# Kernel optimization log

Measured on AMD Instinct MI355X. Metric: run time of the kernel, lower is better.

The kernel has to match this reference:

```python
import jax, jax.numpy as jnp
import numpy as np

N = 50000
E = 1600000
D_IN = 256
D_OUT = 256
NUM_SAMPLES = 5
LN_EPS = 1e-5


def setup_inputs() -> dict:
    key = jax.random.key(0)
    ks = jax.random.split(key, 6)
    x = jax.random.normal(ks[0], (N, D_IN), dtype=jnp.float32)
    adj_indices = jax.random.randint(ks[1], (2, E), 0, N, dtype=jnp.int32)
    adj_values = jax.random.uniform(ks[2], (E,), dtype=jnp.float32)
    mask = jax.random.uniform(ks[3], (NUM_SAMPLES, D_OUT), dtype=jnp.float32)
    # Xavier-uniform init as in reset_parameters
    limit_w = float(np.sqrt(6.0 / (D_IN + D_OUT)))
    weight = jax.random.uniform(ks[4], (D_IN, D_OUT), dtype=jnp.float32,
                                minval=-limit_w, maxval=limit_w)
    limit_b = float(np.sqrt(6.0 / (1 + D_OUT)))
    bias = jax.random.uniform(ks[5], (1, D_OUT), dtype=jnp.float32,
                              minval=-limit_b, maxval=limit_b)
    ln_gamma = jnp.ones((D_OUT,), dtype=jnp.float32)
    ln_beta = jnp.zeros((D_OUT,), dtype=jnp.float32)
    return {"x": x, "adj_indices": adj_indices, "adj_values": adj_values,
            "mask": mask, "weight": weight, "bias": bias,
            "ln_gamma": ln_gamma, "ln_beta": ln_beta}


def reference(x, adj_indices, adj_values, mask, weight, bias, ln_gamma, ln_beta):
    # dense transform: [N, D_in] @ [D_in, D_out]
    h = x @ weight
    # sparse adjacency spmm (COO): out[r] += v_e * h[c] for each edge e=(r,c)
    rows, cols = adj_indices[0], adj_indices[1]
    h = jax.ops.segment_sum(adj_values[:, None] * h[cols], rows, num_segments=N)
    # bias + ELU
    h = jax.nn.elu(h + bias)
    # LayerNorm over feature dim
    mu = jnp.mean(h, axis=-1, keepdims=True)
    var = jnp.var(h, axis=-1, keepdims=True)
    h = (h - mu) * jax.lax.rsqrt(var + LN_EPS) * ln_gamma + ln_beta
    # expand to num_samples and apply per-sample mask: [N, S, D_out]
    out = h[:, None, :] * mask[None, :, :]
    return out
```

## Files before the change

### kernel.cpp

```cpp
#include <hip/hip_runtime.h>
#include <math.h>

#define NNODES 50000
#define D 256
#define NSAMP 5
#define LN_EPS 1e-5f
#define NB 196
#define BCAP 9216
#define ACHUNK 8192

typedef __bf16 bf16;
typedef __attribute__((ext_vector_type(8))) __bf16 bf16x8;
typedef __attribute__((ext_vector_type(4))) float f32x4;
typedef unsigned long long u64;
typedef unsigned int u32;

__device__ inline float bflo(u32 u) { return __uint_as_float(u << 16); }
__device__ inline float bfhi(u32 u) { return __uint_as_float(u & 0xffff0000u); }

__device__ inline u64 packrec(int r, int c, float v) {
    return (u64)(u32)(c | (r << 16)) | ((u64)__float_as_uint(v) << 32);
}

__global__ __launch_bounds__(256) void prep_t_kernel(const float* __restrict__ w,
                                                     bf16* __restrict__ wt) {
    __shared__ float t[64][65];
    const int bi = blockIdx.x >> 2;
    const int bj = blockIdx.x & 3;
    const int tid = threadIdx.x;
#pragma unroll
    for (int it = 0; it < 16; ++it) {
        const int krow = (tid >> 6) + it * 4;
        const int ncol = tid & 63;
        t[krow][ncol] = w[(size_t)(bi * 64 + krow) * D + (bj * 64 + ncol)];
    }
    __syncthreads();
#pragma unroll
    for (int it = 0; it < 16; ++it) {
        const int nrow = (tid >> 6) + it * 4;
        const int kcol = tid & 63;
        wt[(size_t)(bj * 64 + nrow) * D + (bi * 64 + kcol)] = (bf16)t[kcol][nrow];
    }
}

__global__ __launch_bounds__(256) void gemm_binA_kernel(const float* __restrict__ x,
                                                        const bf16* __restrict__ wt,
                                                        bf16* __restrict__ h,
                                                        const int* __restrict__ rows,
                                                        const int* __restrict__ cols,
                                                        const float* __restrict__ vals,
                                                        int* __restrict__ bcur,
                                                        u64* __restrict__ binned,
                                                        int AB, int E) {
    if ((int)blockIdx.x < AB) {
        __shared__ int hist[NB];
        __shared__ int base[NB];
        for (int i = threadIdx.x; i < NB; i += 256) hist[i] = 0;
        __syncthreads();
        const int e0 = blockIdx.x * ACHUNK;
        const int e1 = min(e0 + ACHUNK, E);
        for (int e = e0 + threadIdx.x; e < e1; e += 256)
            atomicAdd(&hist[rows[e] >> 8], 1);
        __syncthreads();
        for (int i = threadIdx.x; i < NB; i += 256) {
            const int c = hist[i];
            base[i] = c ? atomicAdd(&bcur[i], c) : 0;
            hist[i] = 0;
        }
        __syncthreads();
        for (int e = e0 + threadIdx.x; e < e1; e += 256) {
            const int r = rows[e];
            const int b = r >> 8;
            const int k = base[b] + atomicAdd(&hist[b], 1);
            if (k < BCAP)
                binned[(size_t)b * BCAP + k] = packrec(r, cols[e], vals[e]);
        }
        return;
    }

    const int gb = blockIdx.x - AB;
    const int wave = threadIdx.x >> 6;
    const int lane = threadIdx.x & 63;
    const int row0 = gb * 64 + wave * 16;
    const int am = lane & 15;
    const int ag = lane >> 4;

    int arow = row0 + am;
    if (arow >= NNODES) arow = NNODES - 1;

    f32x4 acc[16];
#pragma unroll
    for (int n = 0; n < 16; ++n) acc[n] = (f32x4){0.f, 0.f, 0.f, 0.f};

#pragma unroll
    for (int kk = 0; kk < 8; ++kk) {
        const int kb = kk * 32 + ag * 8;
        const float* xp = x + (size_t)arow * D + kb;
        const f32x4 a0 = __builtin_nontemporal_load((const f32x4*)xp);
        const f32x4 a1 = __builtin_nontemporal_load((const f32x4*)(xp + 4));
        bf16x8 a;
        a[0] = (bf16)a0[0]; a[1] = (bf16)a0[1]; a[2] = (bf16)a0[2]; a[3] = (bf16)a0[3];
        a[4] = (bf16)a1[0]; a[5] = (bf16)a1[1]; a[6] = (bf16)a1[2]; a[7] = (bf16)a1[3];
#pragma unroll
        for (int n = 0; n < 16; ++n) {
            const bf16x8 b = *(const bf16x8*)(wt + (size_t)(n * 16 + am) * D + kb);
            acc[n] = __builtin_amdgcn_mfma_f32_16x16x32_bf16(a, b, acc[n], 0, 0, 0);
        }
    }

    const int drow = row0 + ag * 4;
#pragma unroll
    for (int r = 0; r < 4; ++r) {
        if (drow + r < NNODES) {
            bf16* hp = h + (size_t)(drow + r) * D + am;
#pragma unroll
            for (int n = 0; n < 16; ++n) hp[n * 16] = (bf16)acc[n][r];
        }
    }
}

__global__ __launch_bounds__(256) void sortB_kernel(const u64* __restrict__ binned,
                                                    const int* __restrict__ bcur,
                                                    u32* __restrict__ sorted,
                                                    int* __restrict__ rstart,
                                                    int* __restrict__ rcnt) {
    const int b = blockIdx.x;
    const int tid = threadIdx.x;
    const int cnt_b = min(bcur[b], BCAP);
    const u64* src = binned + (size_t)b * BCAP;

    __shared__ int hist[256];
    __shared__ int scn[256];
    hist[tid] = 0;
    __syncthreads();
    for (int i = tid; i < cnt_b; i += 256)
        atomicAdd(&hist[(int)((src[i] >> 16) & 255)], 1);
    __syncthreads();
    const int v = hist[tid];
    scn[tid] = v;
    __syncthreads();
    for (int d = 1; d < 256; d <<= 1) {
        const int t = (tid >= d) ? scn[tid - d] : 0;
        __syncthreads();
        scn[tid] += t;
        __syncthreads();
    }
    const int excl = scn[tid] - v;
    const int r = b * 256 + tid;
    if (r < NNODES) {
        rstart[r] = b * BCAP + excl;
        rcnt[r]   = v;
    }
    hist[tid] = excl;
    __syncthreads();
    for (int i = tid; i < cnt_b; i += 256) {
        const u64 rec = src[i];
        const int k = atomicAdd(&hist[(int)((rec >> 16) & 255)], 1);
        const float vf = __uint_as_float((u32)(rec >> 32));
        const u32 vb = __float_as_uint((float)(bf16)vf) & 0xffff0000u;
        sorted[(size_t)b * BCAP + k] = (u32)(rec & 0xFFFF) | vb;
    }
}

__global__ __launch_bounds__(256) void row_kernel(const unsigned short* __restrict__ hb,
                                                  const int* __restrict__ rstart,
                                                  const int* __restrict__ rcnt,
                                                  const u32* __restrict__ ep,
                                                  const float* __restrict__ bias,
                                                  const float* __restrict__ gamma,
                                                  const float* __restrict__ beta,
                                                  const float* __restrict__ mask,
                                                  float* __restrict__ out, int n) {
    const int wave = threadIdx.x >> 6;
    const int lane = threadIdx.x & 63;
    const int r = blockIdx.x * 4 + wave;
    if (r >= n) return;

    const int s = rstart[r];
    const int e = s + rcnt[r];

    float a0 = 0.f, a1 = 0.f, a2 = 0.f, a3 = 0.f;
    int i = s;
    for (; i + 3 < e; i += 4) {
        const u32 e0 = ep[i], e1 = ep[i + 1], e2 = ep[i + 2], e3 = ep[i + 3];
        const uint2 q0 = *(const uint2*)(hb + (size_t)(e0 & 0xFFFF) * D + lane * 4);
        const uint2 q1 = *(const uint2*)(hb + (size_t)(e1 & 0xFFFF) * D + lane * 4);
        const uint2 q2 = *(const uint2*)(hb + (size_t)(e2 & 0xFFFF) * D + lane * 4);
        const uint2 q3 = *(const uint2*)(hb + (size_t)(e3 & 0xFFFF) * D + lane * 4);
        const float v0 = bfhi(e0), v1 = bfhi(e1), v2 = bfhi(e2), v3 = bfhi(e3);
        a0 += v0 * bflo(q0.x) + v1 * bflo(q1.x) + v2 * bflo(q2.x) + v3 * bflo(q3.x);
        a1 += v0 * bfhi(q0.x) + v1 * bfhi(q1.x) + v2 * bfhi(q2.x) + v3 * bfhi(q3.x);
        a2 += v0 * bflo(q0.y) + v1 * bflo(q1.y) + v2 * bflo(q2.y) + v3 * bflo(q3.y);
        a3 += v0 * bfhi(q0.y) + v1 * bfhi(q1.y) + v2 * bfhi(q2.y) + v3 * bfhi(q3.y);
    }
    for (; i < e; ++i) {
        const u32 e0 = ep[i];
        const uint2 q0 = *(const uint2*)(hb + (size_t)(e0 & 0xFFFF) * D + lane * 4);
        const float v0 = bfhi(e0);
        a0 += v0 * bflo(q0.x);
        a1 += v0 * bfhi(q0.x);
        a2 += v0 * bflo(q0.y);
        a3 += v0 * bfhi(q0.y);
    }

    const f32x4 b4 = *(const f32x4*)(bias + lane * 4);
    float x0 = a0 + b4[0], x1 = a1 + b4[1], x2 = a2 + b4[2], x3 = a3 + b4[3];
    x0 = x0 > 0.f ? x0 : expm1f(x0);
    x1 = x1 > 0.f ? x1 : expm1f(x1);
    x2 = x2 > 0.f ? x2 : expm1f(x2);
    x3 = x3 > 0.f ? x3 : expm1f(x3);

    float s1 = x0 + x1 + x2 + x3;
    float s2 = x0 * x0 + x1 * x1 + x2 * x2 + x3 * x3;
#pragma unroll
    for (int d = 1; d < 64; d <<= 1) {
        s1 += __shfl_xor(s1, d);
        s2 += __shfl_xor(s2, d);
    }
    const float mu   = s1 * (1.f / 256.f);
    const float var  = s2 * (1.f / 256.f) - mu * mu;
    const float rsig = rsqrtf(var + LN_EPS);

    const f32x4 g4  = *(const f32x4*)(gamma + lane * 4);
    const f32x4 be4 = *(const f32x4*)(beta + lane * 4);
    const float y0 = (x0 - mu) * rsig * g4[0] + be4[0];
    const float y1 = (x1 - mu) * rsig * g4[1] + be4[1];
    const float y2 = (x2 - mu) * rsig * g4[2] + be4[2];
    const float y3 = (x3 - mu) * rsig * g4[3] + be4[3];

#pragma unroll
    for (int smp = 0; smp < NSAMP; ++smp) {
        const f32x4 m4 = *(const f32x4*)(mask + smp * D + lane * 4);
        f32x4 o;
        o[0] = y0 * m4[0];
        o[1] = y1 * m4[1];
        o[2] = y2 * m4[2];
        o[3] = y3 * m4[3];
        __builtin_nontemporal_store(o, (f32x4*)(out + ((size_t)r * NSAMP + smp) * D + lane * 4));
    }
}

extern "C" void kernel_launch(void* const* d_in, const int* in_sizes, int n_in,
                              void* d_out, int out_size, void* d_ws, size_t ws_size,
                              hipStream_t stream) {
    const float* x     = (const float*)d_in[0];
    const int*   adj   = (const int*)d_in[1];
    const float* vals  = (const float*)d_in[2];
    const float* mask  = (const float*)d_in[3];
    const float* w     = (const float*)d_in[4];
    const float* bias  = (const float*)d_in[5];
    const float* gamma = (const float*)d_in[6];
    const float* beta  = (const float*)d_in[7];
    float*       out   = (float*)d_out;

    const int N = NNODES;
    const int E = in_sizes[2];
    const int GB = (N + 63) / 64;
    const int AB = (E + ACHUNK - 1) / ACHUNK;

    char* ws = (char*)d_ws;
    unsigned short* hb     = (unsigned short*)ws;
    u32*            sorted = (u32*)(hb + (size_t)N * D);
    u64*            binned = (u64*)(sorted + (size_t)NB * BCAP);
    bf16*           wt     = (bf16*)(binned + (size_t)NB * BCAP);
    int*            bcur   = (int*)((char*)wt + (size_t)D * D * 2);
    int*            rstart = bcur + 256;
    int*            rcnt   = rstart + N;

    hipMemsetAsync(bcur, 0, 256 * sizeof(int), stream);
    prep_t_kernel<<<16, 256, 0, stream>>>(w, wt);
    gemm_binA_kernel<<<AB + GB, 256, 0, stream>>>(x, wt, (bf16*)hb,
                                                  adj, adj + E, vals, bcur, binned, AB, E);
    sortB_kernel<<<NB, 256, 0, stream>>>(binned, bcur, sorted, rstart, rcnt);
    row_kernel<<<(N + 3) / 4, 256, 0, stream>>>(hb, rstart, rcnt, sorted,
                                                bias, gamma, beta, mask, out, N);
}
```

Baseline: 252.1 us.

## Fuse prep, GEMM/binning and sort into one cooperative persistent kernel

Result: slower. 310.5 us (+23.2%).

```diff
diff --git a/kernel.cpp b/kernel.cpp
--- a/kernel.cpp
+++ b/kernel.cpp
@@ -1,5 +1,8 @@
 #include <hip/hip_runtime.h>
+#include <hip/hip_cooperative_groups.h>
 #include <math.h>
+
+namespace cg = cooperative_groups;
 
 #define NNODES 50000
 #define D 256
@@ -22,63 +25,60 @@
     return (u64)(u32)(c | (r << 16)) | ((u64)__float_as_uint(v) << 32);
 }
 
-__global__ __launch_bounds__(256) void prep_t_kernel(const float* __restrict__ w,
-                                                     bf16* __restrict__ wt) {
+__device__ void dev_prep_unit(int u, const float* __restrict__ w,
+                              bf16* __restrict__ wt, int* __restrict__ bcur) {
     __shared__ float t[64][65];
-    const int bi = blockIdx.x >> 2;
-    const int bj = blockIdx.x & 3;
     const int tid = threadIdx.x;
-#pragma unroll
-    for (int it = 0; it < 16; ++it) {
-        const int krow = (tid >> 6) + it * 4;
-        const int ncol = tid & 63;
-        t[krow][ncol] = w[(size_t)(bi * 64 + krow) * D + (bj * 64 + ncol)];
-    }
-    __syncthreads();
-#pragma unroll
-    for (int it = 0; it < 16; ++it) {
-        const int nrow = (tid >> 6) + it * 4;
-        const int kcol = tid & 63;
-        wt[(size_t)(bj * 64 + nrow) * D + (bi * 64 + kcol)] = (bf16)t[kcol][nrow];
-    }
-}
-
-__global__ __launch_bounds__(256) void gemm_binA_kernel(const float* __restrict__ x,
-                                                        const bf16* __restrict__ wt,
-                                                        bf16* __restrict__ h,
-                                                        const int* __restrict__ rows,
-                                                        const int* __restrict__ cols,
-                                                        const float* __restrict__ vals,
-                                                        int* __restrict__ bcur,
-                                                        u64* __restrict__ binned,
-                                                        int AB, int E) {
-    if ((int)blockIdx.x < AB) {
-        __shared__ int hist[NB];
-        __shared__ int base[NB];
-        for (int i = threadIdx.x; i < NB; i += 256) hist[i] = 0;
-        __syncthreads();
-        const int e0 = blockIdx.x * ACHUNK;
-        const int e1 = min(e0 + ACHUNK, E);
-        for (int e = e0 + threadIdx.x; e < e1; e += 256)
-            atomicAdd(&hist[rows[e] >> 8], 1);
-        __syncthreads();
-        for (int i = threadIdx.x; i < NB; i += 256) {
-            const int c = hist[i];
-            base[i] = c ? atomicAdd(&bcur[i], c) : 0;
-            hist[i] = 0;
+    __syncthreads();
+    if (u < 16) {
+        const int bi = u >> 2, bj = u & 3;
+#pragma unroll
+        for (int it = 0; it < 16; ++it) {
+            const int krow = (tid >> 6) + it * 4;
+            t[krow][tid & 63] = w[(size_t)(bi * 64 + krow) * D + (bj * 64 + (tid & 63))];
         }
         __syncthreads();
-        for (int e = e0 + threadIdx.x; e < e1; e += 256) {
-            const int r = rows[e];
-            const int b = r >> 8;
-            const int k = base[b] + atomicAdd(&hist[b], 1);
-            if (k < BCAP)
-                binned[(size_t)b * BCAP + k] = packrec(r, cols[e], vals[e]);
+#pragma unroll
+        for (int it = 0; it < 16; ++it) {
+            const int nrow = (tid >> 6) + it * 4;
+            wt[(size_t)(bj * 64 + nrow) * D + (bi * 64 + (tid & 63))] = (bf16)t[tid & 63][nrow];
         }
-        return;
-    }
-
-    const int gb = blockIdx.x - AB;
+        __syncthreads();
+    } else {
+        bcur[tid] = 0;
+    }
+}
+
+__device__ void dev_binA(int u, const int* __restrict__ rows, const int* __restrict__ cols,
+                         const float* __restrict__ vals, int* __restrict__ bcur,
+                         u64* __restrict__ binned, int E) {
+    __shared__ int histA[NB];
+    __shared__ int baseA[NB];
+    __syncthreads();
+    for (int i = threadIdx.x; i < NB; i += 256) histA[i] = 0;
+    __syncthreads();
+    const int e0 = u * ACHUNK;
+    const int e1 = min(e0 + ACHUNK, E);
+    for (int e = e0 + threadIdx.x; e < e1; e += 256)
+        atomicAdd(&histA[rows[e] >> 8], 1);
+    __syncthreads();
+    for (int i = threadIdx.x; i < NB; i += 256) {
+        const int c = histA[i];
+        baseA[i] = c ? atomicAdd(&bcur[i], c) : 0;
+        histA[i] = 0;
+    }
+    __syncthreads();
+    for (int e = e0 + threadIdx.x; e < e1; e += 256) {
+        const int r = rows[e];
+        const int b = r >> 8;
+        const int k = baseA[b] + atomicAdd(&histA[b], 1);
+        if (k < BCAP)
+            binned[(size_t)b * BCAP + k] = packrec(r, cols[e], vals[e]);
+    }
+}
+
+__device__ void dev_gemm(int gb, const float* __restrict__ x,
+                         const bf16* __restrict__ wt, bf16* __restrict__ h) {
     const int wave = threadIdx.x >> 6;
     const int lane = threadIdx.x & 63;
     const int row0 = gb * 64 + wave * 16;
@@ -119,47 +119,101 @@
     }
 }
 
-__global__ __launch_bounds__(256) void sortB_kernel(const u64* __restrict__ binned,
-                                                    const int* __restrict__ bcur,
-                                                    u32* __restrict__ sorted,
-                                                    int* __restrict__ rstart,
-                                                    int* __restrict__ rcnt) {
-    const int b = blockIdx.x;
+__device__ void dev_sortB(int b, const u64* __restrict__ binned, const int* __restrict__ bcur,
+                          u32* __restrict__ sorted, int* __restrict__ rstart,
+                          int* __restrict__ rcnt) {
+    __shared__ int histB[256];
+    __shared__ int scnB[256];
     const int tid = threadIdx.x;
+    __syncthreads();
     const int cnt_b = min(bcur[b], BCAP);
     const u64* src = binned + (size_t)b * BCAP;
 
-    __shared__ int hist[256];
-    __shared__ int scn[256];
-    hist[tid] = 0;
+    histB[tid] = 0;
     __syncthreads();
     for (int i = tid; i < cnt_b; i += 256)
-        atomicAdd(&hist[(int)((src[i] >> 16) & 255)], 1);
-    __syncthreads();
-    const int v = hist[tid];
-    scn[tid] = v;
+        atomicAdd(&histB[(int)((src[i] >> 16) & 255)], 1);
+    __syncthreads();
+    const int v = histB[tid];
+    scnB[tid] = v;
     __syncthreads();
     for (int d = 1; d < 256; d <<= 1) {
-        const int t = (tid >= d) ? scn[tid - d] : 0;
+        const int t = (tid >= d) ? scnB[tid - d] : 0;
         __syncthreads();
-        scn[tid] += t;
+        scnB[tid] += t;
         __syncthreads();
     }
-    const int excl = scn[tid] - v;
+    const int excl = scnB[tid] - v;
     const int r = b * 256 + tid;
     if (r < NNODES) {
         rstart[r] = b * BCAP + excl;
         rcnt[r]   = v;
     }
-    hist[tid] = excl;
+    histB[tid] = excl;
     __syncthreads();
     for (int i = tid; i < cnt_b; i += 256) {
         const u64 rec = src[i];
-        const int k = atomicAdd(&hist[(int)((rec >> 16) & 255)], 1);
+        const int k = atomicAdd(&histB[(int)((rec >> 16) & 255)], 1);
         const float vf = __uint_as_float((u32)(rec >> 32));
         const u32 vb = __float_as_uint((float)(bf16)vf) & 0xffff0000u;
         sorted[(size_t)b * BCAP + k] = (u32)(rec & 0xFFFF) | vb;
     }
+}
+
+__global__ __launch_bounds__(256, 2) void mega_kernel(const float* __restrict__ x,
+                                                      const float* __restrict__ w,
+                                                      const int* __restrict__ rows,
+                                                      const int* __restrict__ cols,
+                                                      const float* __restrict__ vals,
+                                                      bf16* __restrict__ wt,
+                                                      int* __restrict__ bcur,
+                                                      u64* __restrict__ binned,
+                                                      u32* __restrict__ sorted,
+                                                      int* __restrict__ rstart,
+                                                      int* __restrict__ rcnt,
+                                                      bf16* __restrict__ h,
+                                                      int E, int AB, int GB) {
+    cg::grid_group grid = cg::this_grid();
+    const int G = gridDim.x;
+
+    for (int u = blockIdx.x; u < 17; u += G)
+        dev_prep_unit(u, w, wt, bcur);
+    grid.sync();
+
+    for (int u = blockIdx.x; u < AB + GB; u += G) {
+        if (u < AB) dev_binA(u, rows, cols, vals, bcur, binned, E);
+        else        dev_gemm(u - AB, x, wt, h);
+    }
+    grid.sync();
+
+    for (int b = blockIdx.x; b < NB; b += G)
+        dev_sortB(b, binned, bcur, sorted, rstart, rcnt);
+}
+
+__global__ __launch_bounds__(256) void fb_prep(const float* __restrict__ w,
+                                               bf16* __restrict__ wt, int* __restrict__ bcur) {
+    dev_prep_unit(blockIdx.x, w, wt, bcur);
+}
+
+__global__ __launch_bounds__(256) void fb_gemm_binA(const float* __restrict__ x,
+                                                    const bf16* __restrict__ wt,
+                                                    bf16* __restrict__ h,
+                                                    const int* __restrict__ rows,
+                                                    const int* __restrict__ cols,
+                                                    const float* __restrict__ vals,
+                                                    int* __restrict__ bcur,
+                                                    u64* __restrict__ binned,
+                                                    int AB, int E) {
+    if ((int)blockIdx.x < AB) dev_binA(blockIdx.x, rows, cols, vals, bcur, binned, E);
+    else                      dev_gemm(blockIdx.x - AB, x, wt, h);
+}
+
+__global__ __launch_bounds__(256) void fb_sortB(const u64* __restrict__ binned,
+                                                const int* __restrict__ bcur,
+                                                u32* __restrict__ sorted,
+                                                int* __restrict__ rstart,
+                                                int* __restrict__ rcnt) {
+    dev_sortB(blockIdx.x, binned, bcur, sorted, rstart, rcnt);
 }
 
 __global__ __launch_bounds__(256) void row_kernel(const unsigned short* __restrict__ hb,
@@ -257,6 +311,8 @@
     const int E = in_sizes[2];
     const int GB = (N + 63) / 64;
     const int AB = (E + ACHUNK - 1) / ACHUNK;
+    const int* rows = adj;
+    const int* cols = adj + E;
 
     char* ws = (char*)d_ws;
     unsigned short* hb     = (unsigned short*)ws;
@@ -266,12 +322,32 @@
     int*            bcur   = (int*)((char*)wt + (size_t)D * D * 2);
     int*            rstart = bcur + 256;
     int*            rcnt   = rstart + N;
-
-    hipMemsetAsync(bcur, 0, 256 * sizeof(int), stream);
-    prep_t_kernel<<<16, 256, 0, stream>>>(w, wt);
-    gemm_binA_kernel<<<AB + GB, 256, 0, stream>>>(x, wt, (bf16*)hb,
-                                                  adj, adj + E, vals, bcur, binned, AB, E);
-    sortB_kernel<<<NB, 256, 0, stream>>>(binned, bcur, sorted, rstart, rcnt);
+    bf16*           hbf    = (bf16*)hb;
+
+    int maxB = 0;
+    hipError_t occ = hipOccupancyMaxActiveBlocksPerMultiprocessor(&maxB, mega_kernel, 256, 0);
+    int G = 512;
+    if (occ == hipSuccess && maxB >= 1) {
+        const long cap = (long)maxB * 256;
+        if (cap < G) G = (int)cap;
+    } else {
+        G = 256;
+    }
+
+    int   Ev = E, ABv = AB, GBv = GB;
+    void* args[] = {(void*)&x, (void*)&w, (void*)&rows, (void*)&cols, (void*)&vals,
+                    (void*)&wt, (void*)&bcur, (void*)&binned, (void*)&sorted,
+                    (void*)&rstart, (void*)&rcnt, (void*)&hbf,
+                    (void*)&Ev, (void*)&ABv, (void*)&GBv};
+
+    hipError_t rc = hipLaunchCooperativeKernel(mega_kernel, dim3(G), dim3(256),
+                                               args, 0, stream);
+    if (rc != hipSuccess) {
+        fb_prep<<<17, 256, 0, stream>>>(w, wt, bcur);
+        fb_gemm_binA<<<AB + GB, 256, 0, stream>>>(x, wt, hbf, rows, cols, vals,
+                                                  bcur, binned, AB, E);
+        fb_sortB<<<NB, 256, 0, stream>>>(binned, bcur, sorted, rstart, rcnt);
+    }
     row_kernel<<<(N + 3) / 4, 256, 0, stream>>>(hb, rstart, rcnt, sorted,
                                                 bias, gamma, beta, mask, out, N);
 }
```

## Regroup kernels: fuse weight prep with binning, GEMM with bin sort

Applied to the files above, without the earlier changes.

Result: faster. 245.6 us, median of 2 (-2.6%).

```diff
diff --git a/kernel.cpp b/kernel.cpp
--- a/kernel.cpp
+++ b/kernel.cpp
@@ -7,7 +7,8 @@
 #define LN_EPS 1e-5f
 #define NB 196
 #define BCAP 9216
-#define ACHUNK 8192
+#define ACHUNK 4096
+#define PREPB 16
 
 typedef __bf16 bf16;
 typedef __attribute__((ext_vector_type(8))) __bf16 bf16x8;
@@ -22,63 +23,107 @@
     return (u64)(u32)(c | (r << 16)) | ((u64)__float_as_uint(v) << 32);
 }
 
-__global__ __launch_bounds__(256) void prep_t_kernel(const float* __restrict__ w,
-                                                     bf16* __restrict__ wt) {
-    __shared__ float t[64][65];
-    const int bi = blockIdx.x >> 2;
-    const int bj = blockIdx.x & 3;
-    const int tid = threadIdx.x;
-#pragma unroll
-    for (int it = 0; it < 16; ++it) {
-        const int krow = (tid >> 6) + it * 4;
-        const int ncol = tid & 63;
-        t[krow][ncol] = w[(size_t)(bi * 64 + krow) * D + (bj * 64 + ncol)];
-    }
-    __syncthreads();
-#pragma unroll
-    for (int it = 0; it < 16; ++it) {
-        const int nrow = (tid >> 6) + it * 4;
-        const int kcol = tid & 63;
-        wt[(size_t)(bj * 64 + nrow) * D + (bi * 64 + kcol)] = (bf16)t[kcol][nrow];
-    }
-}
-
-__global__ __launch_bounds__(256) void gemm_binA_kernel(const float* __restrict__ x,
-                                                        const bf16* __restrict__ wt,
-                                                        bf16* __restrict__ h,
+__global__ __launch_bounds__(512) void prep_binA_kernel(const float* __restrict__ w,
+                                                        bf16* __restrict__ wt,
                                                         const int* __restrict__ rows,
                                                         const int* __restrict__ cols,
                                                         const float* __restrict__ vals,
                                                         int* __restrict__ bcur,
-                                                        u64* __restrict__ binned,
-                                                        int AB, int E) {
-    if ((int)blockIdx.x < AB) {
-        __shared__ int hist[NB];
-        __shared__ int base[NB];
-        for (int i = threadIdx.x; i < NB; i += 256) hist[i] = 0;
-        __syncthreads();
-        const int e0 = blockIdx.x * ACHUNK;
-        const int e1 = min(e0 + ACHUNK, E);
-        for (int e = e0 + threadIdx.x; e < e1; e += 256)
-            atomicAdd(&hist[rows[e] >> 8], 1);
-        __syncthreads();
-        for (int i = threadIdx.x; i < NB; i += 256) {
-            const int c = hist[i];
-            base[i] = c ? atomicAdd(&bcur[i], c) : 0;
-            hist[i] = 0;
-        }
-        __syncthreads();
-        for (int e = e0 + threadIdx.x; e < e1; e += 256) {
-            const int r = rows[e];
-            const int b = r >> 8;
-            const int k = base[b] + atomicAdd(&hist[b], 1);
-            if (k < BCAP)
-                binned[(size_t)b * BCAP + k] = packrec(r, cols[e], vals[e]);
+                                                        u64* __restrict__ binned, int E) {
+    if ((int)blockIdx.x < PREPB) {
+        __shared__ float t[64][65];
+        const int bi = blockIdx.x >> 2;
+        const int bj = blockIdx.x & 3;
+        const int tid = threadIdx.x;
+        const int rr = tid >> 6;
+        const int cc = tid & 63;
+#pragma unroll
+        for (int it = 0; it < 8; ++it) {
+            const int krow = rr + it * 8;
+            t[krow][cc] = w[(size_t)(bi * 64 + krow) * D + (bj * 64 + cc)];
+        }
+        __syncthreads();
+#pragma unroll
+        for (int it = 0; it < 8; ++it) {
+            const int nrow = rr + it * 8;
+            wt[(size_t)(bj * 64 + nrow) * D + (bi * 64 + cc)] = (bf16)t[cc][nrow];
         }
         return;
     }
 
-    const int gb = blockIdx.x - AB;
+    __shared__ int hist[NB];
+    __shared__ int base[NB];
+    for (int i = threadIdx.x; i < NB; i += 512) hist[i] = 0;
+    __syncthreads();
+    const int e0 = (blockIdx.x - PREPB) * ACHUNK;
+    const int e1 = min(e0 + ACHUNK, E);
+    for (int e = e0 + threadIdx.x; e < e1; e += 512)
+        atomicAdd(&hist[rows[e] >> 8], 1);
+    __syncthreads();
+    for (int i = threadIdx.x; i < NB; i += 512) {
+        const int c = hist[i];
+        base[i] = c ? atomicAdd(&bcur[i], c) : 0;
+        hist[i] = 0;
+    }
+    __syncthreads();
+    for (int e = e0 + threadIdx.x; e < e1; e += 512) {
+        const int r = rows[e];
+        const int b = r >> 8;
+        const int k = base[b] + atomicAdd(&hist[b], 1);
+        if (k < BCAP)
+            binned[(size_t)b * BCAP + k] = packrec(r, cols[e], vals[e]);
+    }
+}
+
+__global__ __launch_bounds__(256) void gemm_sortB_kernel(const float* __restrict__ x,
+                                                         const bf16* __restrict__ wt,
+                                                         bf16* __restrict__ h,
+                                                         const u64* __restrict__ binned,
+                                                         const int* __restrict__ bcur,
+                                                         u32* __restrict__ sorted,
+                                                         int* __restrict__ rstart,
+                                                         int* __restrict__ rcnt) {
+    if ((int)blockIdx.x < NB) {
+        const int b = blockIdx.x;
+        const int tid = threadIdx.x;
+        const int cnt_b = min(bcur[b], BCAP);
+        const u64* src = binned + (size_t)b * BCAP;
+
+        __shared__ int hist[256];
+        __shared__ int scn[256];
+        hist[tid] = 0;
+        __syncthreads();
+        for (int i = tid; i < cnt_b; i += 256)
+            atomicAdd(&hist[(int)((src[i] >> 16) & 255)], 1);
+        __syncthreads();
+        const int v = hist[tid];
+        scn[tid] = v;
+        __syncthreads();
+        for (int d = 1; d < 256; d <<= 1) {
+            const int t = (tid >= d) ? scn[tid - d] : 0;
+            __syncthreads();
+            scn[tid] += t;
+            __syncthreads();
+        }
+        const int excl = scn[tid] - v;
+        const int r = b * 256 + tid;
+        if (r < NNODES) {
+            rstart[r] = b * BCAP + excl;
+            rcnt[r]   = v;
+        }
+        hist[tid] = excl;
+        __syncthreads();
+        for (int i = tid; i < cnt_b; i += 256) {
+            const u64 rec = src[i];
+            const int k = atomicAdd(&hist[(int)((rec >> 16) & 255)], 1);
+            const float vf = __uint_as_float((u32)(rec >> 32));
+            const u32 vb = __float_as_uint((float)(bf16)vf) & 0xffff0000u;
+            sorted[(size_t)b * BCAP + k] = (u32)(rec & 0xFFFF) | vb;
+        }
+        return;
+    }
+
+    const int gb = blockIdx.x - NB;
     const int wave = threadIdx.x >> 6;
     const int lane = threadIdx.x & 63;
     const int row0 = gb * 64 + wave * 16;
@@ -116,49 +161,6 @@
 #pragma unroll
             for (int n = 0; n < 16; ++n) hp[n * 16] = (bf16)acc[n][r];
         }
-    }
-}
-
-__global__ __launch_bounds__(256) void sortB_kernel(const u64* __restrict__ binned,
-                                                    const int* __restrict__ bcur,
-                                                    u32* __restrict__ sorted,
-                                                    int* __restrict__ rstart,
-                                                    int* __restrict__ rcnt) {
-    const int b = blockIdx.x;
-    const int tid = threadIdx.x;
-    const int cnt_b = min(bcur[b], BCAP);
-    const u64* src = binned + (size_t)b * BCAP;
-
-    __shared__ int hist[256];
-    __shared__ int scn[256];
-    hist[tid] = 0;
-    __syncthreads();
-    for (int i = tid; i < cnt_b; i += 256)
-        atomicAdd(&hist[(int)((src[i] >> 16) & 255)], 1);
-    __syncthreads();
-    const int v = hist[tid];
-    scn[tid] = v;
-    __syncthreads();
-    for (int d = 1; d < 256; d <<= 1) {
-        const int t = (tid >= d) ? scn[tid - d] : 0;
-        __syncthreads();
-        scn[tid] += t;
-        __syncthreads();
-    }
-    const int excl = scn[tid] - v;
-    const int r = b * 256 + tid;
-    if (r < NNODES) {
-        rstart[r] = b * BCAP + excl;
-        rcnt[r]   = v;
-    }
-    hist[tid] = excl;
-    __syncthreads();
-    for (int i = tid; i < cnt_b; i += 256) {
-        const u64 rec = src[i];
-        const int k = atomicAdd(&hist[(int)((rec >> 16) & 255)], 1);
-        const float vf = __uint_as_float((u32)(rec >> 32));
-        const u32 vb = __float_as_uint((float)(bf16)vf) & 0xffff0000u;
-        sorted[(size_t)b * BCAP + k] = (u32)(rec & 0xFFFF) | vb;
     }
 }
 
@@ -268,10 +270,10 @@
     int*            rcnt   = rstart + N;
 
     hipMemsetAsync(bcur, 0, 256 * sizeof(int), stream);
-    prep_t_kernel<<<16, 256, 0, stream>>>(w, wt);
-    gemm_binA_kernel<<<AB + GB, 256, 0, stream>>>(x, wt, (bf16*)hb,
-                                                  adj, adj + E, vals, bcur, binned, AB, E);
-    sortB_kernel<<<NB, 256, 0, stream>>>(binned, bcur, sorted, rstart, rcnt);
+    prep_binA_kernel<<<PREPB + AB, 512, 0, stream>>>(w, wt, adj, adj + E, vals,
+                                                     bcur, binned, E);
+    gemm_sortB_kernel<<<NB + GB, 256, 0, stream>>>(x, wt, (bf16*)hb,
+                                                   binned, bcur, sorted, rstart, rcnt);
     row_kernel<<<(N + 3) / 4, 256, 0, stream>>>(hb, rstart, rcnt, sorted,
                                                 bias, gamma, beta, mask, out, N);
 }
```
